# Performance work log

Measured on AMD Instinct MI355X. Metric: run time of the kernel, lower is better.

Reference implementation:

```python
import jax, jax.numpy as jnp
import numpy as np

NUM_HEADS = 4

def setup_inputs() -> dict:
    key = jax.random.key(0)
    ks = jax.random.split(key, 8)
    B, L, D, Lc = 4, 4096, 256, 4096
    s = 0.02
    return {
        "x": jax.random.normal(ks[0], (B, L, D), jnp.float32),
        "context": jax.random.normal(ks[1], (B, Lc, D), jnp.float32),
        "Wq": jax.random.normal(ks[2], (D, D), jnp.float32) * s,
        "bq": jax.random.normal(ks[3], (D,), jnp.float32) * s,
        "Wkv": jax.random.normal(ks[4], (D, 2 * D), jnp.float32) * s,
        "bkv": jax.random.normal(ks[5], (2 * D,), jnp.float32) * s,
        "Wp": jax.random.normal(ks[6], (D, D), jnp.float32) * s,
        "bp": jax.random.normal(ks[7], (D,), jnp.float32) * s,
    }


def reference(x, context, Wq, bq, Wkv, bkv, Wp, bp):
    B, L, D = x.shape
    Hn = NUM_HEADS
    hd = D // Hn
    Hs = Ws = int(L ** 0.5)
    scale = hd ** (-0.5)

    # projections
    q = (x @ Wq + bq).reshape(B, L, Hn, hd).transpose(0, 2, 1, 3)        # [B,H,L,hd]
    kv = (context @ Wkv + bkv).reshape(B, -1, 2, Hn, hd)
    k = kv[:, :, 0].transpose(0, 2, 1, 3)                                 # [B,H,Lc,hd]
    v = kv[:, :, 1].transpose(0, 2, 1, 3)                                 # [B,H,Lc,hd]

    attn = jnp.einsum('bhqd,bhkd->bhqk', q, k) * scale                    # [B,H,L,Lc]
    attn_weights = jax.nn.softmax(attn, axis=-1)

    attn_map = attn_weights.mean(axis=1).sum(axis=-1).reshape(B, Hs, Ws)  # [B,H,W]

    out = jnp.einsum('bhqk,bhkd->bhqd', attn_weights, v)                  # [B,H,L,hd]
    out = out.transpose(0, 2, 1, 3).reshape(B, L, D)
    out = out @ Wp + bp
    return (out + x, attn_map)
```

## Files before the change

kernel.cpp:

```cpp
#include <hip/hip_runtime.h>
#include <stdint.h>

typedef unsigned short u16;
typedef short s16x8 __attribute__((ext_vector_type(8)));
typedef u16   u16x8 __attribute__((ext_vector_type(8)));
typedef float f32x4 __attribute__((ext_vector_type(4)));
typedef float f32x16 __attribute__((ext_vector_type(16)));

#define QSCALE 0.180336880111169f

__device__ __forceinline__ u16 f2bf(float f) {
  union { float f; uint32_t u; } v; v.f = f;
  uint32_t r = (v.u + 0x7fffu + ((v.u >> 16) & 1u)) >> 16;
  return (u16)r;
}

__device__ __forceinline__ f32x4 mfma16(s16x8 a, s16x8 b, f32x4 c) {
  return __builtin_amdgcn_mfma_f32_16x16x32_bf16(a, b, c, 0, 0, 0);
}
__device__ __forceinline__ f32x16 mfma32(s16x8 a, s16x8 b, f32x16 c) {
  return __builtin_amdgcn_mfma_f32_32x32x16_bf16(a, b, c, 0, 0, 0);
}

__device__ __forceinline__ void gload16(const void* g, void* l) {
  __builtin_amdgcn_global_load_lds(
      (const __attribute__((address_space(1))) void*)g,
      (__attribute__((address_space(3))) void*)l, 16, 0, 0);
}

__device__ __forceinline__ s16x8 ldsr(const u16* base, int row, int colb) {
  return *(const s16x8*)((const char*)base + row * 128 + (colb ^ ((row & 7) << 4)));
}

__device__ __forceinline__ uint32_t cvtpk(float lo, float hi) {
  uint32_t r;
  asm("v_cvt_pk_bf16_f32 %0, %1, %2" : "=v"(r) : "v"(lo), "v"(hi));
  return r;
}
__device__ __forceinline__ void hswap(uint32_t& a, uint32_t& b) {
  asm("v_permlane32_swap_b32 %0, %1" : "+v"(a), "+v"(b));
}

__global__ void k_convert_in(const float* __restrict__ x, const float* __restrict__ ctx,
                             u16* __restrict__ xb, u16* __restrict__ cb,
                             float* __restrict__ amap) {
  int tid = blockIdx.x * 256 + threadIdx.x;
  const float* src; u16* dst; int off;
  if (tid < 1048576) { src = x;   dst = xb; off = tid * 4; }
  else               { src = ctx; dst = cb; off = (tid - 1048576) * 4; }
  f32x4 v = *(const f32x4*)(src + off);
  u16 o0 = f2bf(v.x), o1 = f2bf(v.y), o2 = f2bf(v.z), o3 = f2bf(v.w);
  u16* d = dst + off;
  d[0] = o0; d[1] = o1; d[2] = o2; d[3] = o3;
  if (tid < 16384) amap[tid] = 1.0f;
}

__global__ void k_convert_w(const float* __restrict__ wq, const float* __restrict__ wkv,
                            const float* __restrict__ wp,
                            u16* __restrict__ wqT, u16* __restrict__ wkvT,
                            u16* __restrict__ wpT) {
  int t = blockIdx.x * 256 + threadIdx.x;
  if (t < 65536) {
    int k = t >> 8, n = t & 255;
    wqT[n * 256 + k] = f2bf(wq[t]);
  } else if (t < 196608) {
    int t2 = t - 65536;
    int k = t2 >> 9, n = t2 & 511;
    wkvT[n * 256 + k] = f2bf(wkv[t2]);
  } else {
    int t2 = t - 196608;
    int k = t2 >> 8, n = t2 & 255;
    wpT[n * 256 + k] = f2bf(wp[t2]);
  }
}

template<int EPI>
__global__ __launch_bounds__(256, 2) void k_gemm(
    const u16* __restrict__ A, const u16* __restrict__ Bt,
    const float* __restrict__ bias, const float* __restrict__ xres,
    u16* __restrict__ o16a, u16* __restrict__ o16b, float* __restrict__ o32) {
  __shared__ u16 Als[2][128 * 64];
  __shared__ u16 Bls[2][64 * 64];
  const int m0 = blockIdx.x * 128;
  const int n0 = blockIdx.y * 64;
  const int tid = threadIdx.x, w = tid >> 6, l = tid & 63;
  const int lr = l & 15, lg = l >> 4;
  const int wm = (w >> 1) * 64, wn = (w & 1) * 32;

  auto stage = [&](int buf, int k0) {
    const char* sa = (const char*)A;
#pragma unroll
    for (int i = 0; i < 4; i++) {
      int dbase = (w * 4 + i) * 1024;
      int d = dbase + l * 16;
      int row = d >> 7, colb = d & 127;
      gload16(sa + (size_t)(m0 + row) * 512 + k0 * 2 + (colb ^ ((row & 7) << 4)),
              (char*)Als[buf] + dbase);
    }
    const char* sb = (const char*)Bt;
#pragma unroll
    for (int i = 0; i < 2; i++) {
      int dbase = (w * 2 + i) * 1024;
      int d = dbase + l * 16;
      int row = d >> 7, colb = d & 127;
      gload16(sb + (size_t)(n0 + row) * 512 + k0 * 2 + (colb ^ ((row & 7) << 4)),
              (char*)Bls[buf] + dbase);
    }
  };

  f32x4 acc[4][2];
#pragma unroll
  for (int i = 0; i < 4; i++)
#pragma unroll
    for (int j = 0; j < 2; j++) acc[i][j] = (f32x4){0.f, 0.f, 0.f, 0.f};

  stage(0, 0);
  __syncthreads();
  int cur = 0;
  for (int ks = 0; ks < 4; ks++) {
    if (ks < 3) stage(cur ^ 1, (ks + 1) * 64);
    s16x8 a[4][2], b[2][2];
#pragma unroll
    for (int mt = 0; mt < 4; mt++)
#pragma unroll
      for (int kf = 0; kf < 2; kf++)
        a[mt][kf] = ldsr(Als[cur], wm + mt * 16 + lr, lg * 16 + kf * 64);
#pragma unroll
    for (int nt = 0; nt < 2; nt++)
#pragma unroll
      for (int kf = 0; kf < 2; kf++)
        b[nt][kf] = ldsr(Bls[cur], wn + nt * 16 + lr, lg * 16 + kf * 64);
#pragma unroll
    for (int mt = 0; mt < 4; mt++)
#pragma unroll
      for (int nt = 0; nt < 2; nt++) {
        acc[mt][nt] = mfma16(a[mt][0], b[nt][0], acc[mt][nt]);
        acc[mt][nt] = mfma16(a[mt][1], b[nt][1], acc[mt][nt]);
      }
    __syncthreads();
    cur ^= 1;
  }

#pragma unroll
  for (int mt = 0; mt < 4; mt++)
#pragma unroll
    for (int nt = 0; nt < 2; nt++)
#pragma unroll
      for (int r = 0; r < 4; r++) {
        int gm = m0 + wm + mt * 16 + lg * 4 + r;
        int gn = n0 + wn + nt * 16 + lr;
        float val = acc[mt][nt][r] + bias[gn];
        if constexpr (EPI == 0) {
          int b_ = gm >> 12, ql = gm & 4095, h = gn >> 6, dd = gn & 63;
          o16a[(((size_t)(b_ * 4 + h) * 4096 + ql) << 6) + dd] = f2bf(val * QSCALE);
        } else if constexpr (EPI == 1) {
          int b_ = gm >> 12, ql = gm & 4095;
          int s = gn >> 8, inner = gn & 255, h = inner >> 6, dd = inner & 63;
          size_t addr = (((size_t)(b_ * 4 + h) * 4096 + ql) << 6) + dd;
          if (s) o16b[addr] = f2bf(val); else o16a[addr] = f2bf(val);
        } else {
          size_t idx = (size_t)gm * 256 + gn;
          o32[idx] = val + xres[idx];
        }
      }
}

__global__ void k_transpose_v(const u16* __restrict__ v, u16* __restrict__ vt) {
  __shared__ u16 tile[64 * 65];
  const int bh = blockIdx.y;
  const int kv0 = blockIdx.x * 64;
  const int tid = threadIdx.x;
  const u16* src = v + ((size_t)bh * 4096 + kv0) * 64;
#pragma unroll
  for (int i = 0; i < 2; i++) {
    int u = (i * 256 + tid) * 8;
    int row = u >> 6, col = u & 63;
    u16x8 val = *(const u16x8*)(src + row * 64 + col);
#pragma unroll
    for (int j = 0; j < 8; j++) tile[row * 65 + col + j] = val[j];
  }
  __syncthreads();
#pragma unroll
  for (int i = 0; i < 2; i++) {
    int u = (i * 256 + tid) * 8;
    int d = u >> 6, kv = u & 63;
    u16x8 o;
#pragma unroll
    for (int j = 0; j < 8; j++) o[j] = tile[(kv + j) * 65 + d];
    *(u16x8*)(vt + ((size_t)bh * 64 + d) * 4096 + kv0 + kv) = o;
  }
}

__global__ __launch_bounds__(256, 2) void k_flash(
    const u16* __restrict__ qb, const u16* __restrict__ kb,
    const u16* __restrict__ vtb, u16* __restrict__ ob) {
  __shared__ u16 kls[3][4096];
  __shared__ u16 vls[3][4096];
  const int id = blockIdx.y * 32 + blockIdx.x;
  const int sw = (id & 7) * 64 + (id >> 3);
  const int bh = sw >> 5;
  const int q0 = (sw & 31) * 128;
  const int tid = threadIdx.x, w = tid >> 6, l = tid & 63;
  const int lr32 = l & 31, hi = l >> 5;
  const char* kbase  = (const char*)(kb + (size_t)bh * 4096 * 64);
  const char* vtbase = (const char*)(vtb + (size_t)bh * 64 * 4096);

  s16x8 qf[4];
  {
    const u16* qp = qb + ((size_t)bh * 4096 + q0 + w * 32 + lr32) * 64 + hi * 8;
#pragma unroll
    for (int mm = 0; mm < 4; mm++) qf[mm] = *(const s16x8*)(qp + mm * 16);
  }
  union { u16 u[8]; s16x8 h; } onesu;
#pragma unroll
  for (int j = 0; j < 8; j++) onesu.u[j] = 0x3f80;

  auto stage = [&](u16* kbuf, u16* vbuf, int t) {
    const char* ks = kbase + (size_t)t * 8192;
#pragma unroll
    for (int i = 0; i < 2; i++) {
      int dbase = (w * 2 + i) * 1024;
      int d = dbase + l * 16;
      int row = d >> 7, colb = d & 127;
      gload16(ks + row * 128 + (colb ^ ((row & 7) << 4)), (char*)kbuf + dbase);
    }
    const char* vs = vtbase + (size_t)t * 128;
#pragma unroll
    for (int i = 0; i < 2; i++) {
      int dbase = (w * 2 + i) * 1024;
      int d = dbase + l * 16;
      int row = d >> 7, colb = d & 127;
      gload16(vs + (size_t)row * 8192 + (colb ^ ((row & 7) << 4)), (char*)vbuf + dbase);
    }
  };

  f32x16 o0, o1, ls;
#pragma unroll
  for (int r = 0; r < 16; r++) { o0[r] = 0.f; o1[r] = 0.f; ls[r] = 0.f; }

  auto pv_block = [&](const f32x16& p, const u16* vbase, int bcol0) {
#pragma unroll
    for (int ks2 = 0; ks2 < 2; ks2++) {
      uint32_t A0 = cvtpk(p[8 * ks2 + 0], p[8 * ks2 + 1]);
      uint32_t A1 = cvtpk(p[8 * ks2 + 2], p[8 * ks2 + 3]);
      uint32_t B0 = cvtpk(p[8 * ks2 + 4], p[8 * ks2 + 5]);
      uint32_t B1 = cvtpk(p[8 * ks2 + 6], p[8 * ks2 + 7]);
      hswap(A0, B0);
      hswap(A1, B1);
      union { uint32_t wv[4]; s16x8 h; } pa;
      pa.wv[0] = A0; pa.wv[1] = A1; pa.wv[2] = B0; pa.wv[3] = B1;
      s16x8 v0 = ldsr(vbase, lr32,      bcol0 + 32 * ks2 + 16 * hi);
      s16x8 v1 = ldsr(vbase, 32 + lr32, bcol0 + 32 * ks2 + 16 * hi);
      __builtin_amdgcn_s_setprio(1);
      o0 = mfma32(pa.h, v0, o0);
      o1 = mfma32(pa.h, v1, o1);
      ls = mfma32(pa.h, onesu.h, ls);
      __builtin_amdgcn_s_setprio(0);
    }
  };

  stage(kls[0], vls[0], 0);
  stage(kls[1], vls[1], 1);
  int cur = 0;
  for (int t = 0; t < 64; t++) {
    if (t < 63) asm volatile("s_waitcnt vmcnt(4)" ::: "memory");
    else        asm volatile("s_waitcnt vmcnt(0)" ::: "memory");
    __builtin_amdgcn_s_barrier();
    asm volatile("" ::: "memory");
    const int stg = (cur == 0) ? 2 : cur - 1;
    if (t < 62) stage(kls[stg], vls[stg], t + 2);
    const u16* kc = kls[cur];
    const u16* vc = vls[cur];
    f32x16 s0, s1;
#pragma unroll
    for (int r = 0; r < 16; r++) { s0[r] = 0.f; s1[r] = 0.f; }
    __builtin_amdgcn_s_setprio(1);
#pragma unroll
    for (int mm = 0; mm < 4; mm++) {
      s16x8 kf0 = ldsr(kc, lr32,      mm * 32 + 16 * hi);
      s16x8 kf1 = ldsr(kc, 32 + lr32, mm * 32 + 16 * hi);
      s0 = mfma32(kf0, qf[mm], s0);
      s1 = mfma32(kf1, qf[mm], s1);
    }
    __builtin_amdgcn_s_setprio(0);
#pragma unroll
    for (int r = 0; r < 16; r++) {
      s0[r] = __builtin_amdgcn_exp2f(s0[r]);
      s1[r] = __builtin_amdgcn_exp2f(s1[r]);
    }
    pv_block(s0, vc, 0);
    pv_block(s1, vc, 64);
    cur = (cur == 2) ? 0 : cur + 1;
  }

  const int b_ = bh >> 2, h = bh & 3;
  u16* obase = ob + (size_t)b_ * 4096 * 256 + h * 64;
#pragma unroll
  for (int r = 0; r < 16; r++) {
    float inv = __builtin_amdgcn_rcpf(ls[r]);
    int qrow = q0 + w * 32 + ((r & 3) + 8 * (r >> 2) + 4 * hi);
    obase[(size_t)qrow * 256 + lr32]      = f2bf(o0[r] * inv);
    obase[(size_t)qrow * 256 + 32 + lr32] = f2bf(o1[r] * inv);
  }
}

extern "C" void kernel_launch(void* const* d_in, const int* in_sizes, int n_in,
                              void* d_out, int out_size, void* d_ws, size_t ws_size,
                              hipStream_t stream) {
  const float* x   = (const float*)d_in[0];
  const float* ctx = (const float*)d_in[1];
  const float* Wq  = (const float*)d_in[2];
  const float* bq  = (const float*)d_in[3];
  const float* Wkv = (const float*)d_in[4];
  const float* bkv = (const float*)d_in[5];
  const float* Wp  = (const float*)d_in[6];
  const float* bp  = (const float*)d_in[7];

  char* ws = (char*)d_ws;
  u16* xb    = (u16*)(ws);
  u16* cb    = (u16*)(ws + 8388608);
  u16* wqT   = (u16*)(ws + 16777216);
  u16* wkvT  = (u16*)(ws + 16908288);
  u16* wpT   = (u16*)(ws + 17170432);
  u16* qbuf  = (u16*)(ws + 17301504);
  u16* kbuf  = (u16*)(ws + 25690112);
  u16* vbuf  = (u16*)(ws + 34078720);
  u16* vtbuf = (u16*)(ws + 42467328);
  u16* aout  = (u16*)(ws + 50855936);
  float* out  = (float*)d_out;
  float* amap = out + 4194304;

  k_convert_in<<<8192, 256, 0, stream>>>(x, ctx, xb, cb, amap);
  k_convert_w<<<1024, 256, 0, stream>>>(Wq, Wkv, Wp, wqT, wkvT, wpT);
  k_gemm<0><<<dim3(128, 4), 256, 0, stream>>>(xb, wqT, bq, nullptr, qbuf, nullptr, nullptr);
  k_gemm<1><<<dim3(128, 8), 256, 0, stream>>>(cb, wkvT, bkv, nullptr, kbuf, vbuf, nullptr);
  k_transpose_v<<<dim3(64, 16), 256, 0, stream>>>(vbuf, vtbuf);
  k_flash<<<dim3(32, 16), 256, 0, stream>>>(qbuf, kbuf, vtbuf, aout);
  k_gemm<2><<<dim3(128, 4), 256, 0, stream>>>(aout, wpT, bp, x, nullptr, nullptr, out);
}
```

Measured before the change: 133.7 us.

## Write V pre-tiled from KV GEMM, load K straight to registers, merge convert kernels

The KV projection epilogue now writes V directly in a 64x64 transposed tiled layout, so the separate transpose kernel and its buffer are gone. The flash kernel no longer stages K through LDS. Each lane loads its K fragments from global memory into double-buffered registers, and only V goes through a 4-deep LDS ring under a new unrolled pipeline with adjusted vmcnt waits. The two convert kernels are merged into one launch. The costs are strided scalar stores in the GEMM epilogue, more register pressure from the K buffers, and possibly less coalesced K reads.

```diff
diff --git a/kernel.cpp b/kernel.cpp
--- a/kernel.cpp
+++ b/kernel.cpp
@@ -41,36 +41,39 @@
   asm("v_permlane32_swap_b32 %0, %1" : "+v"(a), "+v"(b));
 }
 
-__global__ void k_convert_in(const float* __restrict__ x, const float* __restrict__ ctx,
-                             u16* __restrict__ xb, u16* __restrict__ cb,
-                             float* __restrict__ amap) {
+__global__ void k_convert(const float* __restrict__ x, const float* __restrict__ ctx,
+                          const float* __restrict__ wq, const float* __restrict__ wkv,
+                          const float* __restrict__ wp,
+                          u16* __restrict__ xb, u16* __restrict__ cb,
+                          u16* __restrict__ wqT, u16* __restrict__ wkvT,
+                          u16* __restrict__ wpT, float* __restrict__ amap) {
   int tid = blockIdx.x * 256 + threadIdx.x;
-  const float* src; u16* dst; int off;
-  if (tid < 1048576) { src = x;   dst = xb; off = tid * 4; }
-  else               { src = ctx; dst = cb; off = (tid - 1048576) * 4; }
-  f32x4 v = *(const f32x4*)(src + off);
-  u16 o0 = f2bf(v.x), o1 = f2bf(v.y), o2 = f2bf(v.z), o3 = f2bf(v.w);
-  u16* d = dst + off;
-  d[0] = o0; d[1] = o1; d[2] = o2; d[3] = o3;
-  if (tid < 16384) amap[tid] = 1.0f;
-}
-
-__global__ void k_convert_w(const float* __restrict__ wq, const float* __restrict__ wkv,
-                            const float* __restrict__ wp,
-                            u16* __restrict__ wqT, u16* __restrict__ wkvT,
-                            u16* __restrict__ wpT) {
-  int t = blockIdx.x * 256 + threadIdx.x;
-  if (t < 65536) {
-    int k = t >> 8, n = t & 255;
-    wqT[n * 256 + k] = f2bf(wq[t]);
-  } else if (t < 196608) {
-    int t2 = t - 65536;
-    int k = t2 >> 9, n = t2 & 511;
-    wkvT[n * 256 + k] = f2bf(wkv[t2]);
+  if (tid < 2097152) {
+    const float* src; u16* dst; int off;
+    if (tid < 1048576) { src = x;   dst = xb; off = tid * 4; }
+    else               { src = ctx; dst = cb; off = (tid - 1048576) * 4; }
+    f32x4 v = *(const f32x4*)(src + off);
+    u16* d = dst + off;
+    d[0] = f2bf(v.x); d[1] = f2bf(v.y); d[2] = f2bf(v.z); d[3] = f2bf(v.w);
+    if (tid < 16384) amap[tid] = 1.0f;
   } else {
-    int t2 = t - 196608;
-    int k = t2 >> 8, n = t2 & 255;
-    wpT[n * 256 + k] = f2bf(wp[t2]);
+    int t4 = (tid - 2097152) * 4;
+#pragma unroll
+    for (int j = 0; j < 4; j++) {
+      int t = t4 + j;
+      if (t < 65536) {
+        int k = t >> 8, n = t & 255;
+        wqT[n * 256 + k] = f2bf(wq[t]);
+      } else if (t < 196608) {
+        int t2 = t - 65536;
+        int k = t2 >> 9, n = t2 & 511;
+        wkvT[n * 256 + k] = f2bf(wkv[t2]);
+      } else {
+        int t2 = t - 196608;
+        int k = t2 >> 8, n = t2 & 255;
+        wpT[n * 256 + k] = f2bf(wp[t2]);
+      }
+    }
   }
 }
 
@@ -156,8 +159,13 @@
         } else if constexpr (EPI == 1) {
           int b_ = gm >> 12, ql = gm & 4095;
           int s = gn >> 8, inner = gn & 255, h = inner >> 6, dd = inner & 63;
-          size_t addr = (((size_t)(b_ * 4 + h) * 4096 + ql) << 6) + dd;
-          if (s) o16b[addr] = f2bf(val); else o16a[addr] = f2bf(val);
+          if (s) {
+            size_t addr = (((size_t)(b_ * 4 + h) * 64 + (ql >> 6)) * 64 + dd) * 64 + (ql & 63);
+            o16b[addr] = f2bf(val);
+          } else {
+            size_t addr = (((size_t)(b_ * 4 + h) * 4096 + ql) << 6) + dd;
+            o16a[addr] = f2bf(val);
+          }
         } else {
           size_t idx = (size_t)gm * 256 + gn;
           o32[idx] = val + xres[idx];
@@ -165,45 +173,20 @@
       }
 }
 
-__global__ void k_transpose_v(const u16* __restrict__ v, u16* __restrict__ vt) {
-  __shared__ u16 tile[64 * 65];
-  const int bh = blockIdx.y;
-  const int kv0 = blockIdx.x * 64;
-  const int tid = threadIdx.x;
-  const u16* src = v + ((size_t)bh * 4096 + kv0) * 64;
-#pragma unroll
-  for (int i = 0; i < 2; i++) {
-    int u = (i * 256 + tid) * 8;
-    int row = u >> 6, col = u & 63;
-    u16x8 val = *(const u16x8*)(src + row * 64 + col);
-#pragma unroll
-    for (int j = 0; j < 8; j++) tile[row * 65 + col + j] = val[j];
-  }
-  __syncthreads();
-#pragma unroll
-  for (int i = 0; i < 2; i++) {
-    int u = (i * 256 + tid) * 8;
-    int d = u >> 6, kv = u & 63;
-    u16x8 o;
-#pragma unroll
-    for (int j = 0; j < 8; j++) o[j] = tile[(kv + j) * 65 + d];
-    *(u16x8*)(vt + ((size_t)bh * 64 + d) * 4096 + kv0 + kv) = o;
-  }
-}
-
 __global__ __launch_bounds__(256, 2) void k_flash(
     const u16* __restrict__ qb, const u16* __restrict__ kb,
     const u16* __restrict__ vtb, u16* __restrict__ ob) {
-  __shared__ u16 kls[3][4096];
-  __shared__ u16 vls[3][4096];
+  __shared__ u16 vls[4][4096];
   const int id = blockIdx.y * 32 + blockIdx.x;
   const int sw = (id & 7) * 64 + (id >> 3);
   const int bh = sw >> 5;
   const int q0 = (sw & 31) * 128;
   const int tid = threadIdx.x, w = tid >> 6, l = tid & 63;
   const int lr32 = l & 31, hi = l >> 5;
-  const char* kbase  = (const char*)(kb + (size_t)bh * 4096 * 64);
-  const char* vtbase = (const char*)(vtb + (size_t)bh * 64 * 4096);
+  const char* kbase  = (const char*)(kb + (size_t)bh * 262144);
+  const char* vtbase = (const char*)(vtb + (size_t)bh * 262144);
+  const char* kp0 = kbase + lr32 * 128 + hi * 16;
+  const char* kp1 = kp0 + 4096;
 
   s16x8 qf[4];
   {
@@ -215,23 +198,24 @@
 #pragma unroll
   for (int j = 0; j < 8; j++) onesu.u[j] = 0x3f80;
 
-  auto stage = [&](u16* kbuf, u16* vbuf, int t) {
-    const char* ks = kbase + (size_t)t * 8192;
+  auto stageV = [&](int buf, int t) {
 #pragma unroll
     for (int i = 0; i < 2; i++) {
-      int dbase = (w * 2 + i) * 1024;
-      int d = dbase + l * 16;
+      int d = w * 2048 + i * 1024 + l * 16;
       int row = d >> 7, colb = d & 127;
-      gload16(ks + row * 128 + (colb ^ ((row & 7) << 4)), (char*)kbuf + dbase);
-    }
-    const char* vs = vtbase + (size_t)t * 128;
-#pragma unroll
-    for (int i = 0; i < 2; i++) {
-      int dbase = (w * 2 + i) * 1024;
-      int d = dbase + l * 16;
-      int row = d >> 7, colb = d & 127;
-      gload16(vs + (size_t)row * 8192 + (colb ^ ((row & 7) << 4)), (char*)vbuf + dbase);
-    }
+      gload16(vtbase + (size_t)t * 8192 + (d & ~127) + (colb ^ ((row & 7) << 4)),
+              (char*)vls[buf] + d);
+    }
+  };
+
+  s16x8 kA[8], kB[8];
+  auto kload = [&](s16x8 (&kr)[8], int t) {
+#pragma unroll
+    for (int half = 0; half < 2; half++)
+#pragma unroll
+      for (int mm = 0; mm < 4; mm++)
+        kr[half * 4 + mm] =
+            *(const s16x8*)((half ? kp1 : kp0) + (size_t)t * 8192 + mm * 32);
   };
 
   f32x16 o0, o1, ls;
@@ -259,28 +243,15 @@
     }
   };
 
-  stage(kls[0], vls[0], 0);
-  stage(kls[1], vls[1], 1);
-  int cur = 0;
-  for (int t = 0; t < 64; t++) {
-    if (t < 63) asm volatile("s_waitcnt vmcnt(4)" ::: "memory");
-    else        asm volatile("s_waitcnt vmcnt(0)" ::: "memory");
-    __builtin_amdgcn_s_barrier();
-    asm volatile("" ::: "memory");
-    const int stg = (cur == 0) ? 2 : cur - 1;
-    if (t < 62) stage(kls[stg], vls[stg], t + 2);
-    const u16* kc = kls[cur];
-    const u16* vc = vls[cur];
+  auto compute = [&](const s16x8 (&kr)[8], const u16* vc) {
     f32x16 s0, s1;
 #pragma unroll
     for (int r = 0; r < 16; r++) { s0[r] = 0.f; s1[r] = 0.f; }
     __builtin_amdgcn_s_setprio(1);
 #pragma unroll
     for (int mm = 0; mm < 4; mm++) {
-      s16x8 kf0 = ldsr(kc, lr32,      mm * 32 + 16 * hi);
-      s16x8 kf1 = ldsr(kc, 32 + lr32, mm * 32 + 16 * hi);
-      s0 = mfma32(kf0, qf[mm], s0);
-      s1 = mfma32(kf1, qf[mm], s1);
+      s0 = mfma32(kr[mm],     qf[mm], s0);
+      s1 = mfma32(kr[4 + mm], qf[mm], s1);
     }
     __builtin_amdgcn_s_setprio(0);
 #pragma unroll
@@ -290,8 +261,42 @@
     }
     pv_block(s0, vc, 0);
     pv_block(s1, vc, 64);
-    cur = (cur == 2) ? 0 : cur + 1;
-  }
+  };
+
+  stageV(0, 0);
+  stageV(1, 1);
+  kload(kA, 0);
+  for (int tt = 0; tt < 15; tt++) {
+#pragma unroll
+    for (int p = 0; p < 4; p++) {
+      const int t = tt * 4 + p;
+      stageV((p + 2) & 3, t + 2);
+      if (p & 1) kload(kA, t + 1); else kload(kB, t + 1);
+      asm volatile("s_waitcnt vmcnt(10)" ::: "memory");
+      __builtin_amdgcn_s_barrier();
+      asm volatile("" ::: "memory");
+      compute((p & 1) ? kB : kA, vls[p]);
+    }
+  }
+  stageV(2, 62); kload(kB, 61);
+  asm volatile("s_waitcnt vmcnt(10)" ::: "memory");
+  __builtin_amdgcn_s_barrier();
+  asm volatile("" ::: "memory");
+  compute(kA, vls[0]);
+  stageV(3, 63); kload(kA, 62);
+  asm volatile("s_waitcnt vmcnt(10)" ::: "memory");
+  __builtin_amdgcn_s_barrier();
+  asm volatile("" ::: "memory");
+  compute(kB, vls[1]);
+  kload(kB, 63);
+  asm volatile("s_waitcnt vmcnt(8)" ::: "memory");
+  __builtin_amdgcn_s_barrier();
+  asm volatile("" ::: "memory");
+  compute(kA, vls[2]);
+  asm volatile("s_waitcnt vmcnt(0)" ::: "memory");
+  __builtin_amdgcn_s_barrier();
+  asm volatile("" ::: "memory");
+  compute(kB, vls[3]);
 
   const int b_ = bh >> 2, h = bh & 3;
   u16* obase = ob + (size_t)b_ * 4096 * 256 + h * 64;
@@ -324,17 +329,14 @@
   u16* wpT   = (u16*)(ws + 17170432);
   u16* qbuf  = (u16*)(ws + 17301504);
   u16* kbuf  = (u16*)(ws + 25690112);
-  u16* vbuf  = (u16*)(ws + 34078720);
-  u16* vtbuf = (u16*)(ws + 42467328);
-  u16* aout  = (u16*)(ws + 50855936);
+  u16* vtbuf = (u16*)(ws + 34078720);
+  u16* aout  = (u16*)(ws + 42467328);
   float* out  = (float*)d_out;
   float* amap = out + 4194304;
 
-  k_convert_in<<<8192, 256, 0, stream>>>(x, ctx, xb, cb, amap);
-  k_convert_w<<<1024, 256, 0, stream>>>(Wq, Wkv, Wp, wqT, wkvT, wpT);
+  k_convert<<<8448, 256, 0, stream>>>(x, ctx, Wq, Wkv, Wp, xb, cb, wqT, wkvT, wpT, amap);
   k_gemm<0><<<dim3(128, 4), 256, 0, stream>>>(xb, wqT, bq, nullptr, qbuf, nullptr, nullptr);
-  k_gemm<1><<<dim3(128, 8), 256, 0, stream>>>(cb, wkvT, bkv, nullptr, kbuf, vbuf, nullptr);
-  k_transpose_v<<<dim3(64, 16), 256, 0, stream>>>(vbuf, vtbuf);
+  k_gemm<1><<<dim3(128, 8), 256, 0, stream>>>(cb, wkvT, bkv, nullptr, kbuf, vtbuf, nullptr);
   k_flash<<<dim3(32, 16), 256, 0, stream>>>(qbuf, kbuf, vtbuf, aout);
   k_gemm<2><<<dim3(128, 4), 256, 0, stream>>>(aout, wpT, bp, x, nullptr, nullptr, out);
 }
```

Result: slower. 176.4 us (+31.9%).
